# Kernel tuning notes

Hardware: AMD Instinct MI355X
Metric: run time of the kernel (lower is better)

The kernel has to match this reference:

```python
import jax, jax.numpy as jnp
import numpy as np

N, E, F, H, C, K = 50000, 1600000, 256, 6, 16, 40
NEG_SLOPE = 0.2  # PyG GATConv default
EPS = 1e-16


def _gat_layer(x, src, dst, W, a_s, a_d, b, heads, out_ch, concat):
    # linear transform per head: [N, heads, out_ch]
    h = (x @ W).reshape(N, heads, out_ch)
    # per-node attention logits
    al_s = jnp.einsum('nhc,hc->nh', h, a_s)  # source term
    al_d = jnp.einsum('nhc,hc->nh', h, a_d)  # destination term
    # edge-wise score + segment softmax over incoming edges of each dst node
    e = jax.nn.leaky_relu(al_s[src] + al_d[dst], NEG_SLOPE)  # [E', heads]
    m = jax.ops.segment_max(e, dst, num_segments=N)
    ex = jnp.exp(e - m[dst])
    denom = jax.ops.segment_sum(ex, dst, num_segments=N)
    alpha = ex / (denom[dst] + EPS)  # [E', heads]
    # weighted scatter-add aggregation
    out = jax.ops.segment_sum(h[src] * alpha[:, :, None], dst, num_segments=N)
    out = out.reshape(N, heads * out_ch) if concat else out.mean(axis=1)
    return out + b


def setup_inputs() -> dict:
    key = jax.random.key(0)
    ks = jax.random.split(key, 16)
    s = 0.05
    inp = {
        'x': jax.random.normal(ks[0], (N, F), dtype=jnp.float32),
        'edge_index': jax.random.randint(ks[1], (2, E), 0, N, dtype=jnp.int64 if jax.config.jax_enable_x64 else jnp.int32),
        'W1': jax.random.normal(ks[2], (F, H * C), dtype=jnp.float32) * s,
        'a1_s': jax.random.normal(ks[3], (H, C), dtype=jnp.float32) * s,
        'a1_d': jax.random.normal(ks[4], (H, C), dtype=jnp.float32) * s,
        'b1': jnp.zeros((H * C,), dtype=jnp.float32),
        'W2': jax.random.normal(ks[5], (H * C, H * C), dtype=jnp.float32) * s,
        'a2_s': jax.random.normal(ks[6], (H, C), dtype=jnp.float32) * s,
        'a2_d': jax.random.normal(ks[7], (H, C), dtype=jnp.float32) * s,
        'b2': jnp.zeros((H * C,), dtype=jnp.float32),
        'W3': jax.random.normal(ks[8], (H * C, H * C), dtype=jnp.float32) * s,
        'a3_s': jax.random.normal(ks[9], (H, C), dtype=jnp.float32) * s,
        'a3_d': jax.random.normal(ks[10], (H, C), dtype=jnp.float32) * s,
        'b3': jnp.zeros((H * C,), dtype=jnp.float32),
        'W4': jax.random.normal(ks[11], (H * C, K), dtype=jnp.float32) * s,
        'a4_s': jax.random.normal(ks[12], (1, K), dtype=jnp.float32) * s,
        'a4_d': jax.random.normal(ks[13], (1, K), dtype=jnp.float32) * s,
        'b4': jnp.zeros((K,), dtype=jnp.float32),
    }
    return inp


def reference(x, edge_index, W1, a1_s, a1_d, b1, W2, a2_s, a2_d, b2,
              W3, a3_s, a3_d, b3, W4, a4_s, a4_d, b4):
    # PyG GATConv adds self-loops by default
    loops = jnp.arange(N, dtype=edge_index.dtype)
    src = jnp.concatenate([edge_index[0], loops])
    dst = jnp.concatenate([edge_index[1], loops])
    # dropout is identity at eval time
    h = jax.nn.relu(_gat_layer(x, src, dst, W1, a1_s, a1_d, b1, H, C, True))
    h = jax.nn.relu(_gat_layer(h, src, dst, W2, a2_s, a2_d, b2, H, C, True))
    h = jax.nn.relu(_gat_layer(h, src, dst, W3, a3_s, a3_d, b3, H, C, True))
    h = _gat_layer(h, src, dst, W4, a4_s, a4_d, b4, 1, K, False)
    return jax.nn.log_softmax(h, axis=1)
```

## Files before the change

kernel.cpp:

```cpp
#include <hip/hip_runtime.h>
#include <cstdint>
#include <cstddef>

namespace {

constexpr int N  = 50000;
constexpr int E  = 1600000;
constexpr int ET = E + N;
constexpr int F  = 256;
constexpr int H  = 6;
constexpr int C  = 16;
constexpr int HC = H * C;
constexpr int K  = 40;
constexpr int NBUCK = (N + 255) / 256;
constexpr int EPB2  = 8192;
constexpr int HBLK  = (ET + EPB2 - 1) / EPB2;

typedef __attribute__((ext_vector_type(8))) short short8;
typedef __attribute__((ext_vector_type(4))) float f32x4;
typedef __attribute__((ext_vector_type(2))) float f32x2;

__device__ inline uint32_t f2bf(float f) {
  uint32_t u = __float_as_uint(f);
  return (u + 0x7FFFu + ((u >> 16) & 1u)) >> 16;
}
__device__ inline float bflo(uint32_t u) { return __uint_as_float(u << 16); }
__device__ inline float bfhi(uint32_t u) { return __uint_as_float(u & 0xFFFF0000u); }


__global__ void coarse_hist_kernel(const int* __restrict__ ei, int* __restrict__ hist) {
  __shared__ int h[256];
  const int t = threadIdx.x;
  h[t] = 0;
  __syncthreads();
  const int cbase = blockIdx.x * EPB2;
  const int cend = (cbase + EPB2 < ET) ? (cbase + EPB2) : ET;
  for (int e0 = cbase + t * 4; e0 < cend; e0 += 1024) {
    if (e0 + 3 < E && e0 + 3 < cend) {
      int4 dv = *reinterpret_cast<const int4*>(ei + E + e0);
      atomicAdd(&h[dv.x >> 8], 1);
      atomicAdd(&h[dv.y >> 8], 1);
      atomicAdd(&h[dv.z >> 8], 1);
      atomicAdd(&h[dv.w >> 8], 1);
    } else {
#pragma unroll
      for (int q = 0; q < 4; q++) {
        int e = e0 + q;
        if (e < cend) {
          int dd = (e < E) ? ei[E + e] : (e - E);
          atomicAdd(&h[dd >> 8], 1);
        }
      }
    }
  }
  __syncthreads();
  hist[blockIdx.x * 256 + t] = h[t];
}

__global__ void coarse_scan_kernel(const int* __restrict__ hist, int* __restrict__ base,
                                   int* __restrict__ bucket_base, int* __restrict__ rowp) {
  __shared__ int sc[256];
  const int d = threadIdx.x;
  int tot = 0;
#pragma unroll 4
  for (int b = 0; b < HBLK; b++) tot += hist[b * 256 + d];
  sc[d] = tot;
  __syncthreads();
  for (int off = 1; off < 256; off <<= 1) {
    int tv = (d >= off) ? sc[d - off] : 0;
    __syncthreads();
    sc[d] += tv;
    __syncthreads();
  }
  const int excl = sc[d] - tot;
  bucket_base[d] = excl;
  if (d == 255) {
    bucket_base[256] = sc[255];
    rowp[N] = sc[255];
  }
  int run = excl;
#pragma unroll 4
  for (int b = 0; b < HBLK; b++) {
    int v = hist[b * 256 + d];
    base[b * 256 + d] = run;
    run += v;
  }
}

__global__ void coarse_scatter_kernel(const int* __restrict__ ei, const int* __restrict__ base,
                                      uint32_t* __restrict__ keys) {
  __shared__ int cnt[256];
  const int t = threadIdx.x;
  cnt[t] = base[blockIdx.x * 256 + t];
  __syncthreads();
  const int cbase = blockIdx.x * EPB2;
  const int cend = (cbase + EPB2 < ET) ? (cbase + EPB2) : ET;
  for (int e0 = cbase + t * 4; e0 < cend; e0 += 1024) {
    if (e0 + 3 < E && e0 + 3 < cend) {
      int4 dv = *reinterpret_cast<const int4*>(ei + E + e0);
      int4 sv = *reinterpret_cast<const int4*>(ei + e0);
      int p0 = atomicAdd(&cnt[dv.x >> 8], 1);
      keys[p0] = ((uint32_t)dv.x << 16) | (uint32_t)sv.x;
      int p1 = atomicAdd(&cnt[dv.y >> 8], 1);
      keys[p1] = ((uint32_t)dv.y << 16) | (uint32_t)sv.y;
      int p2 = atomicAdd(&cnt[dv.z >> 8], 1);
      keys[p2] = ((uint32_t)dv.z << 16) | (uint32_t)sv.z;
      int p3 = atomicAdd(&cnt[dv.w >> 8], 1);
      keys[p3] = ((uint32_t)dv.w << 16) | (uint32_t)sv.w;
    } else {
#pragma unroll
      for (int q = 0; q < 4; q++) {
        int e = e0 + q;
        if (e < cend) {
          int dd, ssrc;
          if (e < E) { dd = ei[E + e]; ssrc = ei[e]; }
          else       { dd = e - E; ssrc = e - E; }
          int p = atomicAdd(&cnt[dd >> 8], 1);
          keys[p] = ((uint32_t)dd << 16) | (uint32_t)ssrc;
        }
      }
    }
  }
}

__global__ void bucket_sort_kernel(const uint32_t* __restrict__ keys,
                                   const int* __restrict__ bucket_base,
                                   int* __restrict__ rowp, int* __restrict__ col) {
  __shared__ int hist[256];
  __shared__ int sc[256];
  __shared__ int ofs[256];
  const int b = blockIdx.x;
  const int t = threadIdx.x;
  hist[t] = 0;
  __syncthreads();
  const int k0 = bucket_base[b], k1 = bucket_base[b + 1];
  for (int i = k0 + t; i < k1; i += 256)
    atomicAdd(&hist[(keys[i] >> 16) & 255], 1);
  __syncthreads();
  const int v = hist[t];
  sc[t] = v;
  __syncthreads();
  for (int off = 1; off < 256; off <<= 1) {
    int tv = (t >= off) ? sc[t - off] : 0;
    __syncthreads();
    sc[t] += tv;
    __syncthreads();
  }
  ofs[t] = k0 + sc[t] - v;
  const int node = b * 256 + t;
  if (node < N) rowp[node] = ofs[t];
  hist[t] = 0;
  __syncthreads();
  for (int i = k0 + t; i < k1; i += 256) {
    uint32_t key = keys[i];
    int loc = (key >> 16) & 255;
    int p = ofs[loc] + atomicAdd(&hist[loc], 1);
    col[p] = (int)(key & 0xFFFFu);
  }
}


__global__ void tobf16_kernel(const float* __restrict__ src, uint32_t* __restrict__ dst,
                              int n2) {
  int i = blockIdx.x * blockDim.x + threadIdx.x;
  if (i >= n2) return;
  float2 v = reinterpret_cast<const float2*>(src)[i];
  dst[i] = (f2bf(v.y) << 16) | f2bf(v.x);
}


__global__ void cvtW_kernel(const float* __restrict__ W1, const float* __restrict__ W2,
                            const float* __restrict__ W3, const float* __restrict__ W4,
                            uint16_t* __restrict__ WT1, uint16_t* __restrict__ WT2,
                            uint16_t* __restrict__ WT3, uint16_t* __restrict__ WT4) {
  constexpr int T1 = 96 * 256, T2 = 96 * 96, T3 = 96 * 96, T4 = 48 * 96;
  int t = blockIdx.x * blockDim.x + threadIdx.x;
  if (t < T1) {
    int n = t / 256, k = t % 256;
    WT1[t] = (uint16_t)f2bf(W1[(size_t)k * 96 + n]);
  } else if (t < T1 + T2) {
    int u = t - T1; int n = u / 96, k = u % 96;
    WT2[u] = (uint16_t)f2bf(W2[(size_t)k * 96 + n]);
  } else if (t < T1 + T2 + T3) {
    int u = t - T1 - T2; int n = u / 96, k = u % 96;
    WT3[u] = (uint16_t)f2bf(W3[(size_t)k * 96 + n]);
  } else if (t < T1 + T2 + T3 + T4) {
    int u = t - T1 - T2 - T3; int n = u / 96, k = u % 96;
    WT4[u] = (n < K) ? (uint16_t)f2bf(W4[(size_t)k * K + n]) : (uint16_t)0;
  }
}


template <int KD, int NT, int NCOLS, int OST>
__launch_bounds__(256)
__global__ void mfma_gemm_kernel(const uint32_t* __restrict__ A,
                                 const uint16_t* __restrict__ WT,
                                 uint16_t* __restrict__ hOut, int M) {
  constexpr int KU = KD / 2;
  const int wave = threadIdx.x >> 6;
  const int lane = threadIdx.x & 63;
  const int m0 = (blockIdx.x * 4 + wave) * 16;
  if (m0 >= M) return;
  const int r = lane & 15, g = lane >> 4;
  int rowA = m0 + r;
  if (rowA > M - 1) rowA = M - 1;
  const uint32_t* arow = A + (size_t)rowA * KU + g * 4;
  const uint32_t* wt32 = reinterpret_cast<const uint32_t*>(WT);

  f32x4 acc[NT];
#pragma unroll
  for (int nt = 0; nt < NT; nt++) acc[nt] = (f32x4){0.f, 0.f, 0.f, 0.f};

#pragma unroll
  for (int ks = 0; ks < KD / 32; ks++) {
    short8 av = *reinterpret_cast<const short8*>(arow + ks * 16);
#pragma unroll
    for (int nt = 0; nt < NT; nt++) {
      short8 bv = *reinterpret_cast<const short8*>(
          wt32 + (size_t)(nt * 16 + r) * KU + ks * 16 + g * 4);
      acc[nt] = __builtin_amdgcn_mfma_f32_16x16x32_bf16(av, bv, acc[nt], 0, 0, 0);
    }
  }

  const int orow = m0 + g * 4;
#pragma unroll
  for (int nt = 0; nt < NT; nt++) {
    const int ocol = nt * 16 + r;
#pragma unroll
    for (int t = 0; t < 4; t++) {
      int rr = orow + t;
      if (rr < M && ocol < NCOLS)
        hOut[(size_t)rr * OST + ocol] = (uint16_t)f2bf(acc[nt][t]);
    }
  }
}


__global__ void pack_kernel(const uint32_t* __restrict__ hB,
                            const float* __restrict__ as_, const float* __restrict__ ad_,
                            uint32_t* __restrict__ recs, float* __restrict__ aldP) {
  int t = blockIdx.x * 256 + threadIdx.x;
  if (t >= N * H) return;
  int n = t / H, hh = t % H;
  const uint32_t* hp = hB + (size_t)n * 48 + hh * 8;
  float f[16];
  float ss = 0.f, dd = 0.f;
#pragma unroll
  for (int i = 0; i < 8; i++) {
    uint32_t u = hp[i];
    f[2 * i] = bflo(u);
    f[2 * i + 1] = bfhi(u);
  }
#pragma unroll
  for (int c = 0; c < 16; c++) {
    ss += f[c] * as_[hh * 16 + c];
    dd += f[c] * ad_[hh * 16 + c];
  }
  uint32_t* rp = recs + (size_t)n * 32;
#pragma unroll
  for (int q = 0; q < 4; q++) {
    uint32_t w = 0;
    w = (uint32_t)__builtin_amdgcn_cvt_pk_fp8_f32(f[4 * q + 0], f[4 * q + 1], (int)w, false);
    w = (uint32_t)__builtin_amdgcn_cvt_pk_fp8_f32(f[4 * q + 2], f[4 * q + 3], (int)w, true);
    rp[hh * 4 + q] = w;
  }
  rp[24 + hh] = __float_as_uint(ss);
  aldP[(size_t)n * 8 + hh] = dd;
}


__global__ void pack4_kernel(const uint32_t* __restrict__ h4B,
                             const float* __restrict__ as_, const float* __restrict__ ad_,
                             uint32_t* __restrict__ recs4, float* __restrict__ ald4) {
  int n = blockIdx.x * 256 + threadIdx.x;
  if (n >= N) return;
  const uint32_t* hp = h4B + (size_t)n * 32;
  float f[40];
  float ss = 0.f, dd = 0.f;
#pragma unroll
  for (int i = 0; i < 20; i++) {
    uint32_t u = hp[i];
    f[2 * i] = bflo(u);
    f[2 * i + 1] = bfhi(u);
  }
#pragma unroll
  for (int c = 0; c < 40; c++) {
    ss += f[c] * as_[c];
    dd += f[c] * ad_[c];
  }
  uint32_t* rp = recs4 + (size_t)n * 16;
#pragma unroll
  for (int q = 0; q < 10; q++) {
    uint32_t w = 0;
    w = (uint32_t)__builtin_amdgcn_cvt_pk_fp8_f32(f[4 * q + 0], f[4 * q + 1], (int)w, false);
    w = (uint32_t)__builtin_amdgcn_cvt_pk_fp8_f32(f[4 * q + 2], f[4 * q + 3], (int)w, true);
    rp[q] = w;
  }
  rp[10] = __float_as_uint(ss);
  ald4[n] = dd;
}


template <int LPN, int NPW, int REC32, int ALSW, int HDIV, int PAD, bool LSM>
__launch_bounds__(256)
__global__ void flash_agg3_kernel(const uint32_t* __restrict__ recs,
                                  const int* __restrict__ rowp,
                                  const int* __restrict__ col,
                                  const float* __restrict__ aldP,
                                  const float* __restrict__ bias,
                                  uint4* __restrict__ outB4,
                                  float* __restrict__ outF32) {
  const int lane = threadIdx.x & 63;
  const int wave = threadIdx.x >> 6;
  int g = lane / LPN;
  const int li = lane - g * LPN;
  if (g > NPW - 1) g = NPW - 1;
  int n = (blockIdx.x * 4 + wave) * NPW + g;
  if (n > N - 1) n = N - 1;
  const int hh = li / HDIV;
  const float aldv = aldP[(size_t)n * PAD + hh];
  const int b0 = rowp[n];
  const int deg = rowp[n + 1] - b0;

  int km = deg;
#pragma unroll
  for (int off = 32; off > 0; off >>= 1) {
    int o = __shfl_xor(km, off);
    km = (o > km) ? o : km;
  }

  float a0 = 0.f, a1 = 0.f, a2 = 0.f, a3 = 0.f;
  float a4 = 0.f, a5 = 0.f, a6 = 0.f, a7 = 0.f;
  float ss = 0.f;

#pragma unroll 2
  for (int k = 0; k < km; k++) {
    bool valid = (k < deg);
    int j = b0 + (valid ? k : 0);
    int src = col[j];
    const uint32_t* rec = recs + (size_t)src * REC32;
    uint2 u = *reinterpret_cast<const uint2*>(rec + 2 * li);
    float l = __uint_as_float(rec[ALSW + hh]);
    float e = l + aldv;
    e = fmaxf(e, 0.2f * e);
    float p = __expf(e);
    p = valid ? p : 0.f;
    f32x2 c0 = __builtin_amdgcn_cvt_pk_f32_fp8((int)u.x, false);
    f32x2 c1 = __builtin_amdgcn_cvt_pk_f32_fp8((int)u.x, true);
    f32x2 c2 = __builtin_amdgcn_cvt_pk_f32_fp8((int)u.y, false);
    f32x2 c3 = __builtin_amdgcn_cvt_pk_f32_fp8((int)u.y, true);
    a0 += p * c0.x; a1 += p * c0.y;
    a2 += p * c1.x; a3 += p * c1.y;
    a4 += p * c2.x; a5 += p * c2.y;
    a6 += p * c3.x; a7 += p * c3.y;
    ss += p;
  }

  float inv = 1.f / (ss + 1e-16f);

  if (!LSM) {
    float o0 = fmaxf(a0 * inv + bias[8 * li + 0], 0.f);
    float o1 = fmaxf(a1 * inv + bias[8 * li + 1], 0.f);
    float o2 = fmaxf(a2 * inv + bias[8 * li + 2], 0.f);
    float o3 = fmaxf(a3 * inv + bias[8 * li + 3], 0.f);
    float o4 = fmaxf(a4 * inv + bias[8 * li + 4], 0.f);
    float o5 = fmaxf(a5 * inv + bias[8 * li + 5], 0.f);
    float o6 = fmaxf(a6 * inv + bias[8 * li + 6], 0.f);
    float o7 = fmaxf(a7 * inv + bias[8 * li + 7], 0.f);
    uint4 w;
    w.x = (f2bf(o1) << 16) | f2bf(o0);
    w.y = (f2bf(o3) << 16) | f2bf(o2);
    w.z = (f2bf(o5) << 16) | f2bf(o4);
    w.w = (f2bf(o7) << 16) | f2bf(o6);
    outB4[(size_t)n * LPN + li] = w;
  } else {
    bool vl = (li < 5);
    float v0 = vl ? a0 * inv + bias[8 * li + 0] : -1e30f;
    float v1 = vl ? a1 * inv + bias[8 * li + 1] : -1e30f;
    float v2 = vl ? a2 * inv + bias[8 * li + 2] : -1e30f;
    float v3 = vl ? a3 * inv + bias[8 * li + 3] : -1e30f;
    float v4 = vl ? a4 * inv + bias[8 * li + 4] : -1e30f;
    float v5 = vl ? a5 * inv + bias[8 * li + 5] : -1e30f;
    float v6 = vl ? a6 * inv + bias[8 * li + 6] : -1e30f;
    float v7 = vl ? a7 * inv + bias[8 * li + 7] : -1e30f;
    float mx = fmaxf(fmaxf(fmaxf(v0, v1), fmaxf(v2, v3)),
                     fmaxf(fmaxf(v4, v5), fmaxf(v6, v7)));
#pragma unroll
    for (int off = 1; off < 8; off <<= 1) mx = fmaxf(mx, __shfl_xor(mx, off));
    float es = 0.f;
    if (vl)
      es = __expf(v0 - mx) + __expf(v1 - mx) + __expf(v2 - mx) + __expf(v3 - mx) +
           __expf(v4 - mx) + __expf(v5 - mx) + __expf(v6 - mx) + __expf(v7 - mx);
#pragma unroll
    for (int off = 1; off < 8; off <<= 1) es += __shfl_xor(es, off);
    float lse = mx + __logf(es);
    if (vl) {
      float* op = outF32 + (size_t)n * K + li * 8;
      float4 w0 = make_float4(v0 - lse, v1 - lse, v2 - lse, v3 - lse);
      float4 w1 = make_float4(v4 - lse, v5 - lse, v6 - lse, v7 - lse);
      *reinterpret_cast<float4*>(op) = w0;
      *reinterpret_cast<float4*>(op + 4) = w1;
    }
  }
}

inline int cdiv(int a, int b) { return (a + b - 1) / b; }

}

extern "C" void kernel_launch(void* const* d_in, const int* in_sizes, int n_in,
                              void* d_out, int out_size, void* d_ws, size_t ws_size,
                              hipStream_t stream) {
  (void)in_sizes; (void)n_in; (void)out_size; (void)ws_size;
  const float* x   = (const float*)d_in[0];
  const int*   ei  = (const int*)d_in[1];
  const float* W1  = (const float*)d_in[2];
  const float* a1s = (const float*)d_in[3];
  const float* a1d = (const float*)d_in[4];
  const float* b1  = (const float*)d_in[5];
  const float* W2  = (const float*)d_in[6];
  const float* a2s = (const float*)d_in[7];
  const float* a2d = (const float*)d_in[8];
  const float* b2  = (const float*)d_in[9];
  const float* W3  = (const float*)d_in[10];
  const float* a3s = (const float*)d_in[11];
  const float* a3d = (const float*)d_in[12];
  const float* b3  = (const float*)d_in[13];
  const float* W4  = (const float*)d_in[14];
  const float* a4s = (const float*)d_in[15];
  const float* a4d = (const float*)d_in[16];
  const float* b4  = (const float*)d_in[17];
  float* out = (float*)d_out;

  char* ws = (char*)d_ws;
  size_t off = 0;
  auto alloc = [&](size_t bytes) {
    void* p = ws + off;
    off = (off + bytes + 255) & ~(size_t)255;
    return p;
  };
  int*      hist  = (int*)alloc((size_t)HBLK * 256 * 4);
  int*      basep = (int*)alloc((size_t)HBLK * 256 * 4);
  int*      bbase = (int*)alloc((size_t)257 * 4);
  int*      rowp  = (int*)alloc((size_t)(N + 1) * 4);
  uint32_t* keys  = (uint32_t*)alloc((size_t)ET * 4);
  int*      col   = (int*)alloc((size_t)ET * 4);
  uint32_t* xB    = (uint32_t*)alloc((size_t)N * (F / 2) * 4);
  uint16_t* WT1   = (uint16_t*)alloc((size_t)96 * 256 * 2);
  uint16_t* WT2   = (uint16_t*)alloc((size_t)96 * 96 * 2);
  uint16_t* WT3   = (uint16_t*)alloc((size_t)96 * 96 * 2);
  uint16_t* WT4   = (uint16_t*)alloc((size_t)48 * 96 * 2);
  uint32_t* hB    = (uint32_t*)alloc((size_t)N * (HC / 2) * 4);
  uint32_t* actB  = (uint32_t*)alloc((size_t)N * (HC / 2) * 4);
  uint32_t* h4B   = (uint32_t*)alloc((size_t)N * 32 * 4);
  uint32_t* recs  = (uint32_t*)alloc((size_t)N * 32 * 4);
  uint32_t* recs4 = (uint32_t*)alloc((size_t)N * 16 * 4);
  float*    aldP  = (float*)alloc((size_t)N * 8 * 4);

  coarse_hist_kernel<<<HBLK, 256, 0, stream>>>(ei, hist);
  coarse_scan_kernel<<<1, 256, 0, stream>>>(hist, basep, bbase, rowp);
  coarse_scatter_kernel<<<HBLK, 256, 0, stream>>>(ei, basep, keys);
  bucket_sort_kernel<<<NBUCK, 256, 0, stream>>>(keys, bbase, rowp, col);

  tobf16_kernel<<<cdiv(N * (F / 2), 256), 256, 0, stream>>>(x, xB, N * (F / 2));
  cvtW_kernel<<<cdiv(96 * 256 + 96 * 96 * 2 + 48 * 96, 256), 256, 0, stream>>>(
      W1, W2, W3, W4, WT1, WT2, WT3, WT4);

  const int gNH  = cdiv(N * H, 256);
  const int gN1  = cdiv(N, 256);
  const int gG   = cdiv(N, 64);
  const int gA96 = cdiv(N, 20);
  const int gA40 = cdiv(N, 32);

  mfma_gemm_kernel<F, 6, HC, HC><<<gG, 256, 0, stream>>>(xB, WT1, (uint16_t*)hB, N);
  pack_kernel<<<gNH, 256, 0, stream>>>(hB, a1s, a1d, recs, aldP);
  flash_agg3_kernel<12, 5, 32, 24, 2, 8, false><<<gA96, 256, 0, stream>>>(
      recs, rowp, col, aldP, b1, (uint4*)actB, nullptr);

  mfma_gemm_kernel<HC, 6, HC, HC><<<gG, 256, 0, stream>>>(actB, WT2, (uint16_t*)hB, N);
  pack_kernel<<<gNH, 256, 0, stream>>>(hB, a2s, a2d, recs, aldP);
  flash_agg3_kernel<12, 5, 32, 24, 2, 8, false><<<gA96, 256, 0, stream>>>(
      recs, rowp, col, aldP, b2, (uint4*)actB, nullptr);

  mfma_gemm_kernel<HC, 6, HC, HC><<<gG, 256, 0, stream>>>(actB, WT3, (uint16_t*)hB, N);
  pack_kernel<<<gNH, 256, 0, stream>>>(hB, a3s, a3d, recs, aldP);
  flash_agg3_kernel<12, 5, 32, 24, 2, 8, false><<<gA96, 256, 0, stream>>>(
      recs, rowp, col, aldP, b3, (uint4*)actB, nullptr);

  mfma_gemm_kernel<HC, 3, K, 64><<<gG, 256, 0, stream>>>(actB, WT4, (uint16_t*)h4B, N);
  pack4_kernel<<<gN1, 256, 0, stream>>>(h4B, a4s, a4d, recs4, aldP);
  flash_agg3_kernel<8, 8, 16, 10, 16, 1, true><<<gA40, 256, 0, stream>>>(
      recs4, rowp, col, aldP, b4, nullptr, out);
}
```

Before: 316.3 us.

## Fuse GEMM with fp8 record packing and split aggregation into two edge streams

The GEMM for layers 1-3 now stages its fp32 accumulators in shared memory and writes the fp8 feature records and attention logits directly, so the separate pack kernel and the bf16 intermediate buffer are gone. This removes one launch and one round trip through global memory per layer, and the logits are computed from fp32 values instead of bf16-rounded ones. The aggregation kernel now walks two halves of each node's edge list at once with separate accumulators, which doubles the gathers in flight and halves the loop trip count. The cost is more registers in the aggregation kernel, which may lower occupancy, plus a 25 KB shared tile in the GEMM.

```diff
diff --git a/kernel.cpp b/kernel.cpp
--- a/kernel.cpp
+++ b/kernel.cpp
@@ -191,6 +191,77 @@
 }
 
 
+template <int KD>
+__launch_bounds__(256)
+__global__ void gemm_pack_kernel(const uint32_t* __restrict__ A,
+                                 const uint16_t* __restrict__ WT,
+                                 const float* __restrict__ as_,
+                                 const float* __restrict__ ad_,
+                                 uint32_t* __restrict__ recs,
+                                 float* __restrict__ aldP) {
+  constexpr int KU = KD / 2;
+  __shared__ float lds[64][97];
+  const int wave = threadIdx.x >> 6;
+  const int lane = threadIdx.x & 63;
+  const int r = lane & 15, g = lane >> 4;
+  const int m0 = (blockIdx.x * 4 + wave) * 16;
+  int rowA = m0 + r;
+  if (rowA > N - 1) rowA = N - 1;
+  const uint32_t* arow = A + (size_t)rowA * KU + g * 4;
+  const uint32_t* wt32 = reinterpret_cast<const uint32_t*>(WT);
+
+  f32x4 acc[6];
+#pragma unroll
+  for (int nt = 0; nt < 6; nt++) acc[nt] = (f32x4){0.f, 0.f, 0.f, 0.f};
+
+#pragma unroll
+  for (int ks = 0; ks < KD / 32; ks++) {
+    short8 av = *reinterpret_cast<const short8*>(arow + ks * 16);
+#pragma unroll
+    for (int nt = 0; nt < 6; nt++) {
+      short8 bv = *reinterpret_cast<const short8*>(
+          wt32 + (size_t)(nt * 16 + r) * KU + ks * 16 + g * 4);
+      acc[nt] = __builtin_amdgcn_mfma_f32_16x16x32_bf16(av, bv, acc[nt], 0, 0, 0);
+    }
+  }
+
+  const int lr0 = wave * 16 + g * 4;
+#pragma unroll
+  for (int nt = 0; nt < 6; nt++) {
+#pragma unroll
+    for (int t = 0; t < 4; t++) lds[lr0 + t][nt * 16 + r] = acc[nt][t];
+  }
+  __syncthreads();
+
+  const int row = threadIdx.x >> 2;
+  const int q = threadIdx.x & 3;
+  const int grow = blockIdx.x * 64 + row;
+  if (grow < N) {
+    const float* lr = lds[row];
+    uint32_t* rp = recs + (size_t)grow * 32;
+#pragma unroll
+    for (int w = 0; w < 6; w++) {
+      const int c0 = q * 24 + w * 4;
+      uint32_t wv = 0;
+      wv = (uint32_t)__builtin_amdgcn_cvt_pk_fp8_f32(lr[c0], lr[c0 + 1], (int)wv, false);
+      wv = (uint32_t)__builtin_amdgcn_cvt_pk_fp8_f32(lr[c0 + 2], lr[c0 + 3], (int)wv, true);
+      rp[q * 6 + w] = wv;
+    }
+#pragma unroll
+    for (int i = 0; i < 3; i++) {
+      const int d = q * 3 + i;
+      const int hh = d >> 1;
+      const float* av = (d & 1) ? ad_ : as_;
+      float s = 0.f;
+#pragma unroll
+      for (int c = 0; c < 16; c++) s += lr[hh * 16 + c] * av[hh * 16 + c];
+      if (d & 1) aldP[(size_t)grow * 8 + hh] = s;
+      else       rp[24 + hh] = __float_as_uint(s);
+    }
+  }
+}
+
+
 template <int KD, int NT, int NCOLS, int OST>
 __launch_bounds__(256)
 __global__ void mfma_gemm_kernel(const uint32_t* __restrict__ A,
@@ -236,39 +307,6 @@
 }
 
 
-__global__ void pack_kernel(const uint32_t* __restrict__ hB,
-                            const float* __restrict__ as_, const float* __restrict__ ad_,
-                            uint32_t* __restrict__ recs, float* __restrict__ aldP) {
-  int t = blockIdx.x * 256 + threadIdx.x;
-  if (t >= N * H) return;
-  int n = t / H, hh = t % H;
-  const uint32_t* hp = hB + (size_t)n * 48 + hh * 8;
-  float f[16];
-  float ss = 0.f, dd = 0.f;
-#pragma unroll
-  for (int i = 0; i < 8; i++) {
-    uint32_t u = hp[i];
-    f[2 * i] = bflo(u);
-    f[2 * i + 1] = bfhi(u);
-  }
-#pragma unroll
-  for (int c = 0; c < 16; c++) {
-    ss += f[c] * as_[hh * 16 + c];
-    dd += f[c] * ad_[hh * 16 + c];
-  }
-  uint32_t* rp = recs + (size_t)n * 32;
-#pragma unroll
-  for (int q = 0; q < 4; q++) {
-    uint32_t w = 0;
-    w = (uint32_t)__builtin_amdgcn_cvt_pk_fp8_f32(f[4 * q + 0], f[4 * q + 1], (int)w, false);
-    w = (uint32_t)__builtin_amdgcn_cvt_pk_fp8_f32(f[4 * q + 2], f[4 * q + 3], (int)w, true);
-    rp[hh * 4 + q] = w;
-  }
-  rp[24 + hh] = __float_as_uint(ss);
-  aldP[(size_t)n * 8 + hh] = dd;
-}
-
-
 __global__ void pack4_kernel(const uint32_t* __restrict__ h4B,
                              const float* __restrict__ as_, const float* __restrict__ ad_,
                              uint32_t* __restrict__ recs4, float* __restrict__ ald4) {
@@ -303,7 +341,7 @@
 
 template <int LPN, int NPW, int REC32, int ALSW, int HDIV, int PAD, bool LSM>
 __launch_bounds__(256)
-__global__ void flash_agg3_kernel(const uint32_t* __restrict__ recs,
+__global__ void flash_agg4_kernel(const uint32_t* __restrict__ recs,
                                   const int* __restrict__ rowp,
                                   const int* __restrict__ col,
                                   const float* __restrict__ aldP,
@@ -321,8 +359,10 @@
   const float aldv = aldP[(size_t)n * PAD + hh];
   const int b0 = rowp[n];
   const int deg = rowp[n + 1] - b0;
-
-  int km = deg;
+  const int d1 = deg >> 1;
+  const int d2 = deg - d1;
+
+  int km = d2;
 #pragma unroll
   for (int off = 32; off > 0; off >>= 1) {
     int o = __shfl_xor(km, off);
@@ -331,32 +371,50 @@
 
   float a0 = 0.f, a1 = 0.f, a2 = 0.f, a3 = 0.f;
   float a4 = 0.f, a5 = 0.f, a6 = 0.f, a7 = 0.f;
-  float ss = 0.f;
-
-#pragma unroll 2
+  float b0f = 0.f, b1f = 0.f, b2f = 0.f, b3f = 0.f;
+  float b4f = 0.f, b5f = 0.f, b6f = 0.f, b7f = 0.f;
+  float ssA = 0.f, ssB = 0.f;
+
   for (int k = 0; k < km; k++) {
-    bool valid = (k < deg);
-    int j = b0 + (valid ? k : 0);
-    int src = col[j];
-    const uint32_t* rec = recs + (size_t)src * REC32;
-    uint2 u = *reinterpret_cast<const uint2*>(rec + 2 * li);
-    float l = __uint_as_float(rec[ALSW + hh]);
-    float e = l + aldv;
-    e = fmaxf(e, 0.2f * e);
-    float p = __expf(e);
-    p = valid ? p : 0.f;
-    f32x2 c0 = __builtin_amdgcn_cvt_pk_f32_fp8((int)u.x, false);
-    f32x2 c1 = __builtin_amdgcn_cvt_pk_f32_fp8((int)u.x, true);
-    f32x2 c2 = __builtin_amdgcn_cvt_pk_f32_fp8((int)u.y, false);
-    f32x2 c3 = __builtin_amdgcn_cvt_pk_f32_fp8((int)u.y, true);
-    a0 += p * c0.x; a1 += p * c0.y;
-    a2 += p * c1.x; a3 += p * c1.y;
-    a4 += p * c2.x; a5 += p * c2.y;
-    a6 += p * c3.x; a7 += p * c3.y;
-    ss += p;
-  }
-
-  float inv = 1.f / (ss + 1e-16f);
+    const bool vA = (k < d1);
+    const bool vB = (k < d2);
+    const int jA = b0 + (vA ? k : 0);
+    const int jB = b0 + d1 + (vB ? k : 0);
+    const int srcA = col[jA];
+    const int srcB = col[jB];
+    const uint32_t* recA = recs + (size_t)srcA * REC32;
+    const uint32_t* recB = recs + (size_t)srcB * REC32;
+    uint2 uA = *reinterpret_cast<const uint2*>(recA + 2 * li);
+    uint2 uB = *reinterpret_cast<const uint2*>(recB + 2 * li);
+    float lA = __uint_as_float(recA[ALSW + hh]);
+    float lB = __uint_as_float(recB[ALSW + hh]);
+    float eA = lA + aldv; eA = fmaxf(eA, 0.2f * eA);
+    float eB = lB + aldv; eB = fmaxf(eB, 0.2f * eB);
+    float pA = __expf(eA); pA = vA ? pA : 0.f;
+    float pB = __expf(eB); pB = vB ? pB : 0.f;
+    f32x2 cA0 = __builtin_amdgcn_cvt_pk_f32_fp8((int)uA.x, false);
+    f32x2 cA1 = __builtin_amdgcn_cvt_pk_f32_fp8((int)uA.x, true);
+    f32x2 cA2 = __builtin_amdgcn_cvt_pk_f32_fp8((int)uA.y, false);
+    f32x2 cA3 = __builtin_amdgcn_cvt_pk_f32_fp8((int)uA.y, true);
+    f32x2 cB0 = __builtin_amdgcn_cvt_pk_f32_fp8((int)uB.x, false);
+    f32x2 cB1 = __builtin_amdgcn_cvt_pk_f32_fp8((int)uB.x, true);
+    f32x2 cB2 = __builtin_amdgcn_cvt_pk_f32_fp8((int)uB.y, false);
+    f32x2 cB3 = __builtin_amdgcn_cvt_pk_f32_fp8((int)uB.y, true);
+    a0 += pA * cA0.x; a1 += pA * cA0.y;
+    a2 += pA * cA1.x; a3 += pA * cA1.y;
+    a4 += pA * cA2.x; a5 += pA * cA2.y;
+    a6 += pA * cA3.x; a7 += pA * cA3.y;
+    ssA += pA;
+    b0f += pB * cB0.x; b1f += pB * cB0.y;
+    b2f += pB * cB1.x; b3f += pB * cB1.y;
+    b4f += pB * cB2.x; b5f += pB * cB2.y;
+    b6f += pB * cB3.x; b7f += pB * cB3.y;
+    ssB += pB;
+  }
+
+  a0 += b0f; a1 += b1f; a2 += b2f; a3 += b3f;
+  a4 += b4f; a5 += b5f; a6 += b6f; a7 += b7f;
+  float inv = 1.f / (ssA + ssB + 1e-16f);
 
   if (!LSM) {
     float o0 = fmaxf(a0 * inv + bias[8 * li + 0], 0.f);
@@ -450,7 +508,6 @@
   uint16_t* WT2   = (uint16_t*)alloc((size_t)96 * 96 * 2);
   uint16_t* WT3   = (uint16_t*)alloc((size_t)96 * 96 * 2);
   uint16_t* WT4   = (uint16_t*)alloc((size_t)48 * 96 * 2);
-  uint32_t* hB    = (uint32_t*)alloc((size_t)N * (HC / 2) * 4);
   uint32_t* actB  = (uint32_t*)alloc((size_t)N * (HC / 2) * 4);
   uint32_t* h4B   = (uint32_t*)alloc((size_t)N * 32 * 4);
   uint32_t* recs  = (uint32_t*)alloc((size_t)N * 32 * 4);
@@ -466,29 +523,25 @@
   cvtW_kernel<<<cdiv(96 * 256 + 96 * 96 * 2 + 48 * 96, 256), 256, 0, stream>>>(
       W1, W2, W3, W4, WT1, WT2, WT3, WT4);
 
-  const int gNH  = cdiv(N * H, 256);
   const int gN1  = cdiv(N, 256);
   const int gG   = cdiv(N, 64);
   const int gA96 = cdiv(N, 20);
   const int gA40 = cdiv(N, 32);
 
-  mfma_gemm_kernel<F, 6, HC, HC><<<gG, 256, 0, stream>>>(xB, WT1, (uint16_t*)hB, N);
-  pack_kernel<<<gNH, 256, 0, stream>>>(hB, a1s, a1d, recs, aldP);
-  flash_agg3_kernel<12, 5, 32, 24, 2, 8, false><<<gA96, 256, 0, stream>>>(
+  gemm_pack_kernel<F><<<gG, 256, 0, stream>>>(xB, WT1, a1s, a1d, recs, aldP);
+  flash_agg4_kernel<12, 5, 32, 24, 2, 8, false><<<gA96, 256, 0, stream>>>(
       recs, rowp, col, aldP, b1, (uint4*)actB, nullptr);
 
-  mfma_gemm_kernel<HC, 6, HC, HC><<<gG, 256, 0, stream>>>(actB, WT2, (uint16_t*)hB, N);
-  pack_kernel<<<gNH, 256, 0, stream>>>(hB, a2s, a2d, recs, aldP);
-  flash_agg3_kernel<12, 5, 32, 24, 2, 8, false><<<gA96, 256, 0, stream>>>(
+  gemm_pack_kernel<HC><<<gG, 256, 0, stream>>>(actB, WT2, a2s, a2d, recs, aldP);
+  flash_agg4_kernel<12, 5, 32, 24, 2, 8, false><<<gA96, 256, 0, stream>>>(
       recs, rowp, col, aldP, b2, (uint4*)actB, nullptr);
 
-  mfma_gemm_kernel<HC, 6, HC, HC><<<gG, 256, 0, stream>>>(actB, WT3, (uint16_t*)hB, N);
-  pack_kernel<<<gNH, 256, 0, stream>>>(hB, a3s, a3d, recs, aldP);
-  flash_agg3_kernel<12, 5, 32, 24, 2, 8, false><<<gA96, 256, 0, stream>>>(
+  gemm_pack_kernel<HC><<<gG, 256, 0, stream>>>(actB, WT3, a3s, a3d, recs, aldP);
+  flash_agg4_kernel<12, 5, 32, 24, 2, 8, false><<<gA96, 256, 0, stream>>>(
       recs, rowp, col, aldP, b3, (uint4*)actB, nullptr);
 
   mfma_gemm_kernel<HC, 3, K, 64><<<gG, 256, 0, stream>>>(actB, WT4, (uint16_t*)h4B, N);
   pack4_kernel<<<gN1, 256, 0, stream>>>(h4B, a4s, a4d, recs4, aldP);
-  flash_agg3_kernel<8, 8, 16, 10, 16, 1, true><<<gA40, 256, 0, stream>>>(
+  flash_agg4_kernel<8, 8, 16, 10, 16, 1, true><<<gA40, 256, 0, stream>>>(
       recs4, rowp, col, aldP, b4, nullptr, out);
 }
```

Result: faster. 308.5 us (-2.5%).
